# Optimization experiments

Hardware: AMD Instinct MI355X
Metric: run time of the kernel (lower is better)

Reference implementation:

```python
import jax, jax.numpy as jnp
import numpy as np

B, S, D, H, DFF = 2, 2048, 1024, 16, 4096
DK = D // H


def _layer_norm(x, g, b, eps=1e-5):
    mu = jnp.mean(x, axis=-1, keepdims=True)
    var = jnp.mean((x - mu) ** 2, axis=-1, keepdims=True)
    return (x - mu) / jnp.sqrt(var + eps) * g + b


def setup_inputs() -> dict:
    key = jax.random.key(0)
    ks = jax.random.split(key, 12)
    w = lambda k, shape: jax.random.normal(k, shape, jnp.float32) * 0.02
    return {
        "x": jax.random.normal(ks[0], (B, S, D), jnp.float32),
        "mask": jnp.tril(jnp.ones((1, 1, S, S), jnp.int32)),  # causal tgt mask
        "Wq": w(ks[1], (D, D)), "bq": jnp.zeros((D,), jnp.float32),
        "Wk": w(ks[2], (D, D)), "bk": jnp.zeros((D,), jnp.float32),
        "Wv": w(ks[3], (D, D)), "bv": jnp.zeros((D,), jnp.float32),
        "Wo": w(ks[4], (D, D)), "bo": jnp.zeros((D,), jnp.float32),
        "W1": w(ks[5], (D, DFF)), "b1": jnp.zeros((DFF,), jnp.float32),
        "W2": w(ks[6], (DFF, D)), "b2": jnp.zeros((D,), jnp.float32),
        "g1": jnp.ones((D,), jnp.float32), "be1": jnp.zeros((D,), jnp.float32),
        "g2": jnp.ones((D,), jnp.float32), "be2": jnp.zeros((D,), jnp.float32),
    }


def reference(x, mask, Wq, bq, Wk, bk, Wv, bv, Wo, bo, W1, b1, W2, b2, g1, be1, g2, be2):
    b, s, d = x.shape
    h, dk = H, DK
    split = lambda t: t.reshape(b, s, h, dk).transpose(0, 2, 1, 3)  # [b,h,s,dk]
    q = split(x @ Wq + bq)
    k = split(x @ Wk + bk)
    v = split(x @ Wv + bv)
    scores = jnp.einsum("bhqd,bhkd->bhqk", q, k) / jnp.sqrt(jnp.float32(dk))
    # ALiBi: slope_h = (2**(8/H))**-(h+1); bias[h,i,j] = slope_h * (j - i)
    slopes = (2.0 ** (8.0 / h)) ** (-jnp.arange(1, h + 1, dtype=jnp.float32))
    rel = (jnp.arange(s)[None, :] - jnp.arange(s)[:, None]).astype(jnp.float32)
    scores = scores + slopes[:, None, None] * rel[None]  # [1? broadcast b,h,s,s]
    scores = jnp.where(mask == 0, jnp.float32(-1e9), scores)
    probs = jax.nn.softmax(scores, axis=-1)
    attn = jnp.einsum("bhqk,bhkd->bhqd", probs, v)
    attn = attn.transpose(0, 2, 1, 3).reshape(b, s, d) @ Wo + bo
    x = _layer_norm(x + attn, g1, be1)
    ff = jax.nn.relu(x @ W1 + b1) @ W2 + b2
    return _layer_norm(x + ff, g2, be2)
```

## Files before the change

### kernel.cpp

```cpp
#include <hip/hip_runtime.h>
#include <stdint.h>

typedef unsigned short u16;
typedef __bf16 bf16x8 __attribute__((ext_vector_type(8)));
typedef float f32x4 __attribute__((ext_vector_type(4)));
typedef float f32x16 __attribute__((ext_vector_type(16)));
typedef unsigned int uint2v __attribute__((ext_vector_type(2)));

#define S_LEN 2048
#define D_MODEL 1024

struct TrueT  { static constexpr bool value = true;  };
struct FalseT { static constexpr bool value = false; };

__device__ __forceinline__ u16 f2b(float f) {
    uint32_t u = __float_as_uint(f);
    u += 0x7FFFu + ((u >> 16) & 1u);
    return (u16)(u >> 16);
}

__device__ __forceinline__ uint32_t pk2(float a, float b) {
    union { struct { __bf16 l, h; } s; uint32_t u; } c;
    c.s.l = (__bf16)a; c.s.h = (__bf16)b; return c.u;
}

__device__ __forceinline__ float fexp2(float x) {
#if __has_builtin(__builtin_amdgcn_exp2f)
    return __builtin_amdgcn_exp2f(x);
#else
    return exp2f(x);
#endif
}

__device__ __forceinline__ uint2v plswap(uint32_t a, uint32_t b) {
#if __has_builtin(__builtin_amdgcn_permlane32_swap)
    return __builtin_amdgcn_permlane32_swap(a, b, false, false);
#else
    uint2v r;
    uint32_t pa = (uint32_t)__shfl_xor((int)a, 32, 64);
    uint32_t pb = (uint32_t)__shfl_xor((int)b, 32, 64);
    const int hi = (threadIdx.x & 63) >> 5;
    r[0] = hi ? pb : a;
    r[1] = hi ? b : pa;
    return r;
#endif
}
__device__ __forceinline__ float xhalf_max(float x) {
    uint2v r = plswap(__float_as_uint(x), __float_as_uint(x));
    return fmaxf(__uint_as_float(r[0]), __uint_as_float(r[1]));
}
__device__ __forceinline__ float xhalf_add(float x) {
    uint2v r = plswap(__float_as_uint(x), __float_as_uint(x));
    return __uint_as_float(r[0]) + __uint_as_float(r[1]);
}

__device__ __forceinline__ void gl16(const void* g, void* l) {
    __builtin_amdgcn_global_load_lds(
        (const __attribute__((address_space(1))) void*)g,
        (__attribute__((address_space(3))) void*)l, 16, 0, 0);
}

__global__ __launch_bounds__(256) void k_convert_bf16(
    const float* __restrict__ in, u16* __restrict__ out, int n)
{
    int i = (blockIdx.x * 256 + threadIdx.x) * 4;
    if (i >= n) return;
    float4 v = *reinterpret_cast<const float4*>(in + i);
    ushort4 o;
    o.x = f2b(v.x); o.y = f2b(v.y); o.z = f2b(v.z); o.w = f2b(v.w);
    *reinterpret_cast<ushort4*>(out + i) = o;
}

__global__ __launch_bounds__(256) void k_transpose_w(
    const float* __restrict__ W, u16* __restrict__ WT, int K, int N)
{
    __shared__ float tile[32][33];
    const int nt = blockIdx.x, kt = blockIdx.y;
    const int tx = threadIdx.x & 31, ty = threadIdx.x >> 5;
#pragma unroll
    for (int i = 0; i < 4; ++i)
        tile[ty + i * 8][tx] = W[(long)(kt * 32 + ty + i * 8) * N + nt * 32 + tx];
    __syncthreads();
#pragma unroll
    for (int i = 0; i < 4; ++i)
        WT[(long)(nt * 32 + ty + i * 8) * K + kt * 32 + tx] = f2b(tile[tx][ty + i * 8]);
}

template <int MODE>
__global__ __launch_bounds__(256) void k_gemm(
    const u16* __restrict__ A, const u16* __restrict__ BT,
    const float* __restrict__ bias, const float* __restrict__ bias2,
    const float* __restrict__ bias3,
    u16* __restrict__ outb, float* __restrict__ outf,
    int M, int N, int K, int va, int vb)
{
    __shared__ u16 As[2][128 * 32];
    __shared__ u16 Bs[2][128 * 32];
    const int t = threadIdx.x;
    const int lane = t & 63, wid = t >> 6;
    const int wm = wid >> 1, wn = wid & 1;
    const int lr = lane & 15, lg = lane >> 4;

    const int GX = gridDim.x, GY = gridDim.y;
    const int dd = blockIdx.y * GX + blockIdx.x;
    const int xcd = dd & 7, ii = dd >> 3;
    const int hb = GY / va, wb = GX / vb;
    const int pr = xcd / vb, pc = xcd % vb;
    const int by = pr * hb + ii / wb;
    const int bx = pc * wb + ii % wb;
    const int m0 = by * 128, n0 = bx * 128;

    const int Kc = K / (int)gridDim.z;
    const long koff = (long)blockIdx.z * Kc;

    f32x4 acc[4][4];
#pragma unroll
    for (int i = 0; i < 4; ++i)
#pragma unroll
        for (int j = 0; j < 4; ++j) acc[i][j] = (f32x4){0.f, 0.f, 0.f, 0.f};

    const int r0 = t >> 2;
    const int ce = (t & 3) * 8;
    const u16* pA0 = A + (long)(m0 + r0) * K + ce + koff;
    const u16* pA1 = A + (long)(m0 + r0 + 64) * K + ce + koff;
    const u16* pB0 = BT + (long)(n0 + r0) * K + ce + koff;
    const u16* pB1 = BT + (long)(n0 + r0 + 64) * K + ce + koff;

    auto STAGE = [&](int buf, int k0) {
        u16* aw = &As[buf][wid * 512];
        u16* bw = &Bs[buf][wid * 512];
        gl16(pA0 + k0, aw);
        gl16(pA1 + k0, aw + 2048);
        gl16(pB0 + k0, bw);
        gl16(pB1 + k0, bw + 2048);
    };

    STAGE(0, 0);
    __syncthreads();
    int cur = 0;
    for (int k0 = 0; k0 < Kc; k0 += 32) {
        if (k0 + 32 < Kc) STAGE(cur ^ 1, k0 + 32);
        bf16x8 af[4], bfr[4];
#pragma unroll
        for (int i = 0; i < 4; ++i)
            af[i] = *reinterpret_cast<const bf16x8*>(&As[cur][(wm * 64 + i * 16 + lr) * 32 + lg * 8]);
#pragma unroll
        for (int j = 0; j < 4; ++j)
            bfr[j] = *reinterpret_cast<const bf16x8*>(&Bs[cur][(wn * 64 + j * 16 + lr) * 32 + lg * 8]);
#pragma unroll
        for (int i = 0; i < 4; ++i)
#pragma unroll
            for (int j = 0; j < 4; ++j)
                acc[i][j] = __builtin_amdgcn_mfma_f32_16x16x32_bf16(af[i], bfr[j], acc[i][j], 0, 0, 0);
        __syncthreads();
        cur ^= 1;
    }

    const long zoff = (long)blockIdx.z * M * N;
#pragma unroll
    for (int i = 0; i < 4; ++i) {
#pragma unroll
        for (int j = 0; j < 4; ++j) {
            const int n = n0 + wn * 64 + j * 16 + lr;
            float bn = 0.f;
            if (MODE == 0)
                bn = (n < 1024) ? bias[n] : (n < 2048) ? bias2[n - 1024] : bias3[n - 2048];
            else if (MODE == 2)
                bn = bias[n];
#pragma unroll
            for (int r = 0; r < 4; ++r) {
                const int m = m0 + wm * 64 + i * 16 + lg * 4 + r;
                float v = acc[i][j][r] + bn;
                if (MODE == 0) {
                    const int b = m >> 11, s = m & 2047;
                    const int which = n >> 10, nn = n & 1023;
                    const int h = nn >> 6, dk = nn & 63;
                    const long bhb = (long)(b * 16 + h) * (2048L * 64);
                    const int s32 = s >> 5, sr = s & 31;
                    long addr;
                    if (which < 2) {
                        addr = bhb + (long)s32 * 2048 + (dk >> 4) * 512 +
                               ((dk >> 3) & 1) * 256 + sr * 8 + (dk & 7);
                    } else {
                        addr = bhb + (long)s32 * 2048 + (dk >> 5) * 1024 +
                               ((sr >> 4) & 1) * 512 + ((sr >> 3) & 1) * 256 +
                               (dk & 31) * 8 + (sr & 7);
                    }
                    outb[(long)which * (32L * 2048 * 64) + addr] = f2b(v);
                } else if (MODE == 2) {
                    outb[(long)m * N + n] = f2b(fmaxf(v, 0.f));
                } else {
                    outf[zoff + (long)m * N + n] = v;
                }
            }
        }
    }
}

__global__ __launch_bounds__(512, 2) void k_gemm8(
    const u16* __restrict__ A, const u16* __restrict__ BT,
    const float* __restrict__ bias, u16* __restrict__ outb,
    int M, int N, int K, int va, int vb)
{
    __shared__ u16 As[2][2][8192];
    __shared__ u16 Bs[2][2][8192];
    const int t = threadIdx.x;
    const int lane = t & 63, wid = t >> 6;
    const int wm = wid >> 2, wn = wid & 3;
    const int lr = lane & 15, lg = lane >> 4;

    const int GX = gridDim.x, GY = gridDim.y;
    const int dd = blockIdx.y * GX + blockIdx.x;
    const int xcd = dd & 7, ii = dd >> 3;
    const int hb = GY / va, wb = GX / vb;
    const int by = (xcd / vb) * hb + ii / wb;
    const int bx = (xcd % vb) * wb + ii % wb;
    const int m0 = by * 256, n0 = bx * 256;

    const int NT = K >> 6;

    auto STAGEU = [&](const u16* __restrict__ P, int rbase, u16* lds_unit,
                      int tt, int kh) {
        const int ko = tt * 64 + kh * 32;
#pragma unroll
        for (int s = 0; s < 2; ++s) {
            const int c = wid * 64 + lane + s * 512;
            const int op = c * 16;
            const int row = op >> 6;
            const int kg = ((op >> 4) & 3) ^ (row & 3);
            gl16(P + (long)(rbase + row) * K + ko + kg * 8,
                 (char*)lds_unit + op);
        }
    };
    auto RD = [&](const u16* unit, int rb) -> bf16x8 {
        const int row = rb + lr;
        const int op = (row * 64 + lg * 16) ^ ((row & 3) << 4);
        return *reinterpret_cast<const bf16x8*>((const char*)unit + op);
    };

    f32x4 acc[8][4];
#pragma unroll
    for (int i = 0; i < 8; ++i)
#pragma unroll
        for (int j = 0; j < 4; ++j) acc[i][j] = (f32x4){0.f, 0.f, 0.f, 0.f};

    STAGEU(A, m0, &As[0][0][0], 0, 0);
    STAGEU(BT, n0, &Bs[0][0][0], 0, 0);
    STAGEU(A, m0, &As[0][1][0], 0, 1);
    STAGEU(BT, n0, &Bs[0][1][0], 0, 1);
    STAGEU(A, m0, &As[1][0][0], 1, 0);
    STAGEU(BT, n0, &Bs[1][0][0], 1, 0);
    asm volatile("s_waitcnt vmcnt(0)" ::: "memory");
    __builtin_amdgcn_s_barrier();

    for (int tt = 0; tt < NT; ++tt) {
        const int sl = tt & 1;
        bf16x8 af[4], bfr[4];

#pragma unroll
        for (int rf = 0; rf < 4; ++rf)
            af[rf] = RD(&As[sl][0][0], wm * 128 + rf * 16);
#pragma unroll
        for (int cf = 0; cf < 4; ++cf)
            bfr[cf] = RD(&Bs[sl][0][0], wn * 64 + cf * 16);
        if (tt + 1 < NT) STAGEU(A, m0, &As[sl ^ 1][1][0], tt + 1, 1);
        __builtin_amdgcn_s_setprio(1);
#pragma unroll
        for (int cf = 0; cf < 4; ++cf)
#pragma unroll
            for (int rf = 0; rf < 4; ++rf)
                acc[rf][cf] = __builtin_amdgcn_mfma_f32_16x16x32_bf16(af[rf], bfr[cf], acc[rf][cf], 0, 0, 0);
        __builtin_amdgcn_s_setprio(0);
        __builtin_amdgcn_s_barrier();

#pragma unroll
        for (int rf = 0; rf < 4; ++rf)
            af[rf] = RD(&As[sl][0][0], wm * 128 + 64 + rf * 16);
        if (tt + 1 < NT) STAGEU(BT, n0, &Bs[sl ^ 1][1][0], tt + 1, 1);
        __builtin_amdgcn_s_setprio(1);
#pragma unroll
        for (int cf = 0; cf < 4; ++cf)
#pragma unroll
            for (int rf = 0; rf < 4; ++rf)
                acc[4 + rf][cf] = __builtin_amdgcn_mfma_f32_16x16x32_bf16(af[rf], bfr[cf], acc[4 + rf][cf], 0, 0, 0);
        __builtin_amdgcn_s_setprio(0);
        asm volatile("s_waitcnt vmcnt(8)" ::: "memory");
        __builtin_amdgcn_s_barrier();

#pragma unroll
        for (int rf = 0; rf < 4; ++rf)
            af[rf] = RD(&As[sl][1][0], wm * 128 + rf * 16);
#pragma unroll
        for (int cf = 0; cf < 4; ++cf)
            bfr[cf] = RD(&Bs[sl][1][0], wn * 64 + cf * 16);
        if (tt + 2 < NT) STAGEU(A, m0, &As[sl][0][0], tt + 2, 0);
        __builtin_amdgcn_s_setprio(1);
#pragma unroll
        for (int cf = 0; cf < 4; ++cf)
#pragma unroll
            for (int rf = 0; rf < 4; ++rf)
                acc[rf][cf] = __builtin_amdgcn_mfma_f32_16x16x32_bf16(af[rf], bfr[cf], acc[rf][cf], 0, 0, 0);
        __builtin_amdgcn_s_setprio(0);
        __builtin_amdgcn_s_barrier();

#pragma unroll
        for (int rf = 0; rf < 4; ++rf)
            af[rf] = RD(&As[sl][1][0], wm * 128 + 64 + rf * 16);
        if (tt + 2 < NT) STAGEU(BT, n0, &Bs[sl][0][0], tt + 2, 0);
        __builtin_amdgcn_s_setprio(1);
#pragma unroll
        for (int cf = 0; cf < 4; ++cf)
#pragma unroll
            for (int rf = 0; rf < 4; ++rf)
                acc[4 + rf][cf] = __builtin_amdgcn_mfma_f32_16x16x32_bf16(af[rf], bfr[cf], acc[4 + rf][cf], 0, 0, 0);
        __builtin_amdgcn_s_setprio(0);
        asm volatile("s_waitcnt vmcnt(8)" ::: "memory");
        __builtin_amdgcn_s_barrier();
    }

#pragma unroll
    for (int fr = 0; fr < 8; ++fr)
#pragma unroll
        for (int cf = 0; cf < 4; ++cf) {
            const int n = n0 + wn * 64 + cf * 16 + lr;
            const float bn = bias[n];
#pragma unroll
            for (int r = 0; r < 4; ++r) {
                const int m = m0 + wm * 128 + fr * 16 + lg * 4 + r;
                outb[(long)m * N + n] = f2b(fmaxf(acc[fr][cf][r] + bn, 0.f));
            }
        }
}

__global__ __launch_bounds__(256, 3) void k_attn4(
    const u16* __restrict__ qg, const u16* __restrict__ kg,
    const u16* __restrict__ vtg, u16* __restrict__ attnb)
{
    __shared__ float Ol[4][32][68];
    __shared__ float Ml[4][32];
    __shared__ float Ll[4][32];

    const int t = threadIdx.x;
    const int lane = t & 63, w = t >> 6;
    const int qc = lane & 31, hi = lane >> 5;
    const int bid = blockIdx.x;
    const int xcd = bid & 7, slot = bid >> 3;
    const int bh = xcd * 4 + (slot & 3);
    const int pr = slot >> 2;
    const int b = bh >> 4, h = bh & 15;
    const float slope2 = fexp2(-0.5f * (float)(h + 1)) * 1.44269504f;
    const float SC = 0.18033688f;
    const long base = (long)bh * (S_LEN * 64L);

    const u16* kptr = kg + base + lane * 8;
    const u16* vptr = vtg + base + lane * 8;
    const u16* qptr = qg + base + lane * 8;

#define LOADK(S, DST) {                                                   \
        const u16* kr_ = kptr + (long)(S) * 2048;                         \
        DST[0] = *reinterpret_cast<const bf16x8*>(kr_);                   \
        DST[1] = *reinterpret_cast<const bf16x8*>(kr_ + 512);             \
        DST[2] = *reinterpret_cast<const bf16x8*>(kr_ + 1024);            \
        DST[3] = *reinterpret_cast<const bf16x8*>(kr_ + 1536); }

    for (int pi = 0; pi < 2; ++pi) {
        const int qt = pi ? pr : 63 - pr;
        const int q_abs = qt * 32 + qc;

        bf16x8 qf[4];
        {
            const u16* qt_ = qptr + (long)qt * 2048;
#pragma unroll
            for (int ds = 0; ds < 4; ++ds)
                qf[ds] = *reinterpret_cast<const bf16x8*>(qt_ + ds * 512);
        }

        f32x16 oacc[2];
#pragma unroll
        for (int i = 0; i < 16; ++i) { oacc[0][i] = 0.f; oacc[1][i] = 0.f; }
        float m = -1e30f, l = 0.f;

        const int nsub = qt + 1;
        const int L = (nsub + 3) >> 2;
        const int s_beg = w * L;
        const int s_end = min(s_beg + L, nsub);
        const bool has_diag = (s_beg < s_end) && (s_end == nsub);
        const int e_un = has_diag ? s_end - 1 : s_end;

        bf16x8 kf[4];

        auto SUBTILE = [&](int s, int nxt, auto MASKC) {
            constexpr bool MASK = decltype(MASKC)::value;
            const int k0 = s * 32;
            f32x16 st;
#pragma unroll
            for (int i = 0; i < 16; ++i) st[i] = 0.f;
#pragma unroll
            for (int ds = 0; ds < 4; ++ds)
                st = __builtin_amdgcn_mfma_f32_32x32x16_bf16(kf[ds], qf[ds], st, 0, 0, 0);
            if (nxt >= 0) LOADK(nxt, kf);
            bf16x8 vf[2][2];
            {
                const u16* vt_ = vptr + (long)s * 2048;
#pragma unroll
                for (int dh = 0; dh < 2; ++dh)
#pragma unroll
                    for (int ks = 0; ks < 2; ++ks)
                        vf[dh][ks] = *reinterpret_cast<const bf16x8*>(
                            vt_ + dh * 1024 + ks * 512);
            }

            const float b0 = slope2 * (float)(k0 - q_abs + 4 * hi);
#pragma unroll
            for (int r = 0; r < 16; ++r) {
                const int roff = (r & 3) + 8 * (r >> 2);
                float xx = fmaf(st[r], SC, fmaf((float)roff, slope2, b0));
                if (MASK) {
                    const int kabs = k0 + roff + 4 * hi;
                    xx = (kabs > q_abs) ? -1e30f : xx;
                }
                st[r] = xx;
            }
            float mt[8];
#pragma unroll
            for (int r = 0; r < 8; ++r) mt[r] = fmaxf(st[2 * r], st[2 * r + 1]);
#pragma unroll
            for (int r = 0; r < 4; ++r) mt[r] = fmaxf(mt[r], mt[r + 4]);
            mt[0] = fmaxf(mt[0], mt[2]); mt[1] = fmaxf(mt[1], mt[3]);
            float mloc = xhalf_max(fmaxf(mt[0], mt[1]));

            if (!__all(mloc <= m + 11.5416f)) {
                const float mnew = fmaxf(m, mloc);
                const float corr = fexp2(m - mnew);
                m = mnew;
                l *= corr;
#pragma unroll
                for (int i = 0; i < 16; ++i) { oacc[0][i] *= corr; oacc[1][i] *= corr; }
            }

#pragma unroll
            for (int r = 0; r < 16; ++r) st[r] = fexp2(st[r] - m);
            float pt[8];
#pragma unroll
            for (int r = 0; r < 8; ++r) pt[r] = st[2 * r] + st[2 * r + 1];
#pragma unroll
            for (int r = 0; r < 4; ++r) pt[r] = pt[r] + pt[r + 4];
            pt[0] += pt[2]; pt[1] += pt[3];
            l += xhalf_add(pt[0] + pt[1]);

            bf16x8 pa[2];
#pragma unroll
            for (int g2 = 0; g2 < 2; ++g2) {
                uint32_t o0 = pk2(st[8 * g2 + 0], st[8 * g2 + 1]);
                uint32_t o1 = pk2(st[8 * g2 + 2], st[8 * g2 + 3]);
                uint32_t o2 = pk2(st[8 * g2 + 4], st[8 * g2 + 5]);
                uint32_t o3 = pk2(st[8 * g2 + 6], st[8 * g2 + 7]);
                uint2v ra = plswap(o0, o2);
                uint2v rb = plswap(o1, o3);
                union { uint32_t wd[4]; bf16x8 v; } c;
                c.wd[0] = ra[0]; c.wd[1] = rb[0]; c.wd[2] = ra[1]; c.wd[3] = rb[1];
                pa[g2] = c.v;
            }
#pragma unroll
            for (int ks = 0; ks < 2; ++ks)
#pragma unroll
                for (int dh = 0; dh < 2; ++dh)
                    oacc[dh] = __builtin_amdgcn_mfma_f32_32x32x16_bf16(vf[dh][ks], pa[ks], oacc[dh], 0, 0, 0);
        };

        int s = s_beg;
        if (s < s_end) LOADK(s, kf);
        for (; s < e_un; ++s)
            SUBTILE(s, (s + 1 < s_end) ? s + 1 : -1, FalseT{});
        if (has_diag)
            SUBTILE(qt, -1, TrueT{});

#pragma unroll
        for (int dh = 0; dh < 2; ++dh)
#pragma unroll
            for (int g = 0; g < 4; ++g) {
                float4 o4 = make_float4(oacc[dh][4 * g + 0], oacc[dh][4 * g + 1],
                                        oacc[dh][4 * g + 2], oacc[dh][4 * g + 3]);
                *reinterpret_cast<float4*>(&Ol[w][qc][dh * 32 + g * 8 + hi * 4]) = o4;
            }
        if (hi == 0) { Ml[w][qc] = m; Ll[w][qc] = l; }
        __syncthreads();

        {
            const int q = t >> 3, dg = t & 7;
            const float m0v = Ml[0][q], m1v = Ml[1][q], m2v = Ml[2][q], m3v = Ml[3][q];
            const float M = fmaxf(fmaxf(m0v, m1v), fmaxf(m2v, m3v));
            float wgt[4];
            wgt[0] = fexp2(m0v - M); wgt[1] = fexp2(m1v - M);
            wgt[2] = fexp2(m2v - M); wgt[3] = fexp2(m3v - M);
            const float lsum = wgt[0] * Ll[0][q] + wgt[1] * Ll[1][q] +
                               wgt[2] * Ll[2][q] + wgt[3] * Ll[3][q];
            float acc8[8];
#pragma unroll
            for (int e = 0; e < 8; ++e) acc8[e] = 0.f;
#pragma unroll
            for (int w4 = 0; w4 < 4; ++w4) {
                const float wg = wgt[w4];
#pragma unroll
                for (int e = 0; e < 8; ++e)
                    acc8[e] += wg * Ol[w4][q][dg * 8 + e];
            }
            const float inv = 1.0f / lsum;
            u16 ob[8];
#pragma unroll
            for (int e = 0; e < 8; ++e) ob[e] = f2b(acc8[e] * inv);
            *reinterpret_cast<uint4*>(
                &attnb[((long)b * S_LEN + qt * 32 + q) * 1024 + h * 64 + dg * 8]) =
                *reinterpret_cast<uint4*>(&ob[0]);
        }
        __syncthreads();
    }
#undef LOADK
}

__global__ __launch_bounds__(256) void k_ln(
    const float* __restrict__ P0, const float* __restrict__ P1,
    const float* __restrict__ resid, const float* __restrict__ pbias,
    const float* __restrict__ g, const float* __restrict__ be,
    float* __restrict__ outf, u16* __restrict__ outb, int writeb)
{
    __shared__ float red[2][4];
    const int row = blockIdx.x, t = threadIdx.x;
    const long o = (long)row * 1024 + t * 4;
    float4 a0 = *reinterpret_cast<const float4*>(P0 + o);
    float4 a1 = *reinterpret_cast<const float4*>(P1 + o);
    float4 rr = *reinterpret_cast<const float4*>(resid + o);
    float4 pb = *reinterpret_cast<const float4*>(pbias + t * 4);
    float4 vv;
    vv.x = a0.x + a1.x + rr.x + pb.x;
    vv.y = a0.y + a1.y + rr.y + pb.y;
    vv.z = a0.z + a1.z + rr.z + pb.z;
    vv.w = a0.w + a1.w + rr.w + pb.w;
    float s = vv.x + vv.y + vv.z + vv.w;
    float sq = vv.x * vv.x + vv.y * vv.y + vv.z * vv.z + vv.w * vv.w;
#pragma unroll
    for (int off = 1; off < 64; off <<= 1) {
        s += __shfl_xor(s, off, 64);
        sq += __shfl_xor(sq, off, 64);
    }
    const int w = t >> 6;
    if ((t & 63) == 0) { red[0][w] = s; red[1][w] = sq; }
    __syncthreads();
    s = red[0][0] + red[0][1] + red[0][2] + red[0][3];
    sq = red[1][0] + red[1][1] + red[1][2] + red[1][3];
    const float mu = s * (1.f / 1024.f);
    const float var = sq * (1.f / 1024.f) - mu * mu;
    const float rs = rsqrtf(var + 1e-5f);
    float4 gv = *reinterpret_cast<const float4*>(&g[t * 4]);
    float4 bv = *reinterpret_cast<const float4*>(&be[t * 4]);
    float4 ov;
    ov.x = (vv.x - mu) * rs * gv.x + bv.x;
    ov.y = (vv.y - mu) * rs * gv.y + bv.y;
    ov.z = (vv.z - mu) * rs * gv.z + bv.z;
    ov.w = (vv.w - mu) * rs * gv.w + bv.w;
    *reinterpret_cast<float4*>(&outf[o]) = ov;
    if (writeb) {
        ushort4 ob;
        ob.x = f2b(ov.x); ob.y = f2b(ov.y); ob.z = f2b(ov.z); ob.w = f2b(ov.w);
        *reinterpret_cast<ushort4*>(&outb[o]) = ob;
    }
}

extern "C" void kernel_launch(void* const* d_in, const int* in_sizes, int n_in,
                              void* d_out, int out_size, void* d_ws, size_t ws_size,
                              hipStream_t stream)
{
    const float* x  = (const float*)d_in[0];
    const float* Wq = (const float*)d_in[2];  const float* bq = (const float*)d_in[3];
    const float* Wk = (const float*)d_in[4];  const float* bk = (const float*)d_in[5];
    const float* Wv = (const float*)d_in[6];  const float* bv = (const float*)d_in[7];
    const float* Wo = (const float*)d_in[8];  const float* bo = (const float*)d_in[9];
    const float* W1 = (const float*)d_in[10]; const float* b1 = (const float*)d_in[11];
    const float* W2 = (const float*)d_in[12]; const float* b2 = (const float*)d_in[13];
    const float* g1 = (const float*)d_in[14]; const float* be1 = (const float*)d_in[15];
    const float* g2 = (const float*)d_in[16]; const float* be2 = (const float*)d_in[17];
    float* out = (float*)d_out;

    char* ws = (char*)d_ws;
    const size_t MB = 1 << 20;
    u16* XB   = (u16*)(ws + 0 * MB);
    u16* QKVT = (u16*)(ws + 8 * MB);
    u16* WOT  = (u16*)(ws + 14 * MB);
    u16* W1T  = (u16*)(ws + 16 * MB);
    u16* W2T  = (u16*)(ws + 96 * MB);
    u16* QKV  = (u16*)(ws + 32 * MB);
    u16* AT   = (u16*)(ws + 64 * MB);
    float* OP = (float*)(ws + 32 * MB);
    float* Y1 = (float*)(ws + 0 * MB);
    u16* Y1B  = (u16*)(ws + 64 * MB);
    u16* Hb   = (u16*)(ws + 24 * MB);
    float* FP = (float*)(ws + 56 * MB);

    u16* Qb = QKV;
    u16* Kb = QKV + 32L * 2048 * 64;
    u16* Vb = QKV + 2 * 32L * 2048 * 64;

    dim3 blk(256);

    k_convert_bf16<<<dim3(4096), blk, 0, stream>>>(x, XB, 4096 * 1024);
    k_transpose_w<<<dim3(32, 32), blk, 0, stream>>>(Wq, QKVT, 1024, 1024);
    k_transpose_w<<<dim3(32, 32), blk, 0, stream>>>(Wk, QKVT + 1024L * 1024, 1024, 1024);
    k_transpose_w<<<dim3(32, 32), blk, 0, stream>>>(Wv, QKVT + 2048L * 1024, 1024, 1024);
    k_transpose_w<<<dim3(32, 32), blk, 0, stream>>>(Wo, WOT, 1024, 1024);
    k_transpose_w<<<dim3(128, 32), blk, 0, stream>>>(W1, W1T, 1024, 4096);
    k_transpose_w<<<dim3(32, 128), blk, 0, stream>>>(W2, W2T, 4096, 1024);

    k_gemm<0><<<dim3(24, 32), blk, 0, stream>>>(XB, QKVT, bq, bk, bv,
                                                QKV, nullptr, 4096, 3072, 1024, 4, 2);

    k_attn4<<<dim3(1024), blk, 0, stream>>>(Qb, Kb, Vb, AT);

    k_gemm<1><<<dim3(8, 32, 2), blk, 0, stream>>>(AT, WOT, nullptr, nullptr, nullptr,
                                                  nullptr, OP, 4096, 1024, 1024, 4, 2);
    k_ln<<<dim3(4096), blk, 0, stream>>>(OP, OP + 4096L * 1024, x, bo,
                                         g1, be1, Y1, Y1B, 1);
    k_gemm8<<<dim3(16, 16), dim3(512), 0, stream>>>(Y1B, W1T, b1, Hb,
                                                    4096, 4096, 1024, 2, 4);
    k_gemm<1><<<dim3(8, 32, 2), blk, 0, stream>>>(Hb, W2T, nullptr, nullptr, nullptr,
                                                  nullptr, FP, 4096, 1024, 4096, 4, 2);
    k_ln<<<dim3(4096), blk, 0, stream>>>(FP, FP + 4096L * 1024, Y1, b2,
                                         g2, be2, out, nullptr, 0);
}
```

Measured before the change: 234.1 us.

## Add 512-thread split-K GEMM with 256x128 tiles for output and FFN2 projections

Introduces k_gemm8n, a 512-thread, 8-wave GEMM with 256x128 block tiles and split-K over gridDim.z that writes fp32 partials, and uses it for the Wo and W2 projections in place of the 256-thread k_gemm<1>. It also changes the LDS swizzle in k_gemm8 from row&3 to (row>>1)&3 to reduce bank conflicts on the 64-byte row layout. The goal is better MFMA utilisation and latency hiding for the N=1024 GEMMs. The trade-off is fewer, larger blocks (256 total) and higher register and LDS use per block.

```diff
diff --git a/kernel.cpp b/kernel.cpp
--- a/kernel.cpp
+++ b/kernel.cpp
@@ -227,14 +227,14 @@
             const int c = wid * 64 + lane + s * 512;
             const int op = c * 16;
             const int row = op >> 6;
-            const int kg = ((op >> 4) & 3) ^ (row & 3);
+            const int kg = ((op >> 4) & 3) ^ ((row >> 1) & 3);
             gl16(P + (long)(rbase + row) * K + ko + kg * 8,
                  (char*)lds_unit + op);
         }
     };
     auto RD = [&](const u16* unit, int rb) -> bf16x8 {
         const int row = rb + lr;
-        const int op = (row * 64 + lg * 16) ^ ((row & 3) << 4);
+        const int op = (row * 64 + lg * 16) ^ (((row >> 1) & 3) << 4);
         return *reinterpret_cast<const bf16x8*>((const char*)unit + op);
     };
 
@@ -328,6 +328,127 @@
             for (int r = 0; r < 4; ++r) {
                 const int m = m0 + wm * 128 + fr * 16 + lg * 4 + r;
                 outb[(long)m * N + n] = f2b(fmaxf(acc[fr][cf][r] + bn, 0.f));
+            }
+        }
+}
+
+__global__ __launch_bounds__(512, 2) void k_gemm8n(
+    const u16* __restrict__ A, const u16* __restrict__ BT,
+    float* __restrict__ outf, int M, int N, int K, int va, int vb)
+{
+    __shared__ u16 As[2][2][8192];
+    __shared__ u16 Bs[2][2][4096];
+    const int t = threadIdx.x;
+    const int lane = t & 63, wid = t >> 6;
+    const int wm = wid >> 1, wn = wid & 1;
+    const int lr = lane & 15, lg = lane >> 4;
+
+    const int GX = gridDim.x, GY = gridDim.y;
+    const int dd = blockIdx.y * GX + blockIdx.x;
+    const int xcd = dd & 7, ii = dd >> 3;
+    const int hb = GY / va, wb = GX / vb;
+    const int by = (xcd / vb) * hb + ii / wb;
+    const int bx = (xcd % vb) * wb + ii % wb;
+    const int m0 = by * 256, n0 = bx * 128;
+
+    const int Kc = K / (int)gridDim.z;
+    const long koff = (long)blockIdx.z * Kc;
+    const int NT = Kc >> 6;
+
+    auto STAGEA = [&](u16* lds_unit, int tt, int kh) {
+        const int ko = tt * 64 + kh * 32;
+#pragma unroll
+        for (int s = 0; s < 2; ++s) {
+            const int c = wid * 64 + lane + s * 512;
+            const int op = c * 16;
+            const int row = op >> 6;
+            const int kg = ((op >> 4) & 3) ^ ((row >> 1) & 3);
+            gl16(A + (long)(m0 + row) * K + koff + ko + kg * 8,
+                 (char*)lds_unit + op);
+        }
+    };
+    auto STAGEB = [&](u16* lds_unit, int tt, int kh) {
+        const int ko = tt * 64 + kh * 32;
+        const int c = wid * 64 + lane;
+        const int op = c * 16;
+        const int row = op >> 6;
+        const int kg = ((op >> 4) & 3) ^ ((row >> 1) & 3);
+        gl16(BT + (long)(n0 + row) * K + koff + ko + kg * 8,
+             (char*)lds_unit + op);
+    };
+    auto RD = [&](const u16* unit, int rb) -> bf16x8 {
+        const int row = rb + lr;
+        const int op = (row * 64 + lg * 16) ^ (((row >> 1) & 3) << 4);
+        return *reinterpret_cast<const bf16x8*>((const char*)unit + op);
+    };
+
+    f32x4 acc[4][4];
+#pragma unroll
+    for (int i = 0; i < 4; ++i)
+#pragma unroll
+        for (int j = 0; j < 4; ++j) acc[i][j] = (f32x4){0.f, 0.f, 0.f, 0.f};
+
+    STAGEA(&As[0][0][0], 0, 0); STAGEB(&Bs[0][0][0], 0, 0);
+    STAGEA(&As[0][1][0], 0, 1); STAGEB(&Bs[0][1][0], 0, 1);
+    STAGEA(&As[1][0][0], 1, 0); STAGEB(&Bs[1][0][0], 1, 0);
+    asm volatile("s_waitcnt vmcnt(0)" ::: "memory");
+    __builtin_amdgcn_s_barrier();
+
+    for (int tt = 0; tt < NT; ++tt) {
+        const int sl = tt & 1;
+        bf16x8 af[4], bfr[4];
+
+#pragma unroll
+        for (int rf = 0; rf < 4; ++rf)
+            af[rf] = RD(&As[sl][0][0], wm * 64 + rf * 16);
+#pragma unroll
+        for (int cf = 0; cf < 4; ++cf)
+            bfr[cf] = RD(&Bs[sl][0][0], wn * 64 + cf * 16);
+        if (tt + 1 < NT) {
+            STAGEA(&As[sl ^ 1][1][0], tt + 1, 1);
+            STAGEB(&Bs[sl ^ 1][1][0], tt + 1, 1);
+        }
+        __builtin_amdgcn_s_setprio(1);
+#pragma unroll
+        for (int cf = 0; cf < 4; ++cf)
+#pragma unroll
+            for (int rf = 0; rf < 4; ++rf)
+                acc[rf][cf] = __builtin_amdgcn_mfma_f32_16x16x32_bf16(af[rf], bfr[cf], acc[rf][cf], 0, 0, 0);
+        __builtin_amdgcn_s_setprio(0);
+        asm volatile("s_waitcnt vmcnt(6)" ::: "memory");
+        __builtin_amdgcn_s_barrier();
+
+#pragma unroll
+        for (int rf = 0; rf < 4; ++rf)
+            af[rf] = RD(&As[sl][1][0], wm * 64 + rf * 16);
+#pragma unroll
+        for (int cf = 0; cf < 4; ++cf)
+            bfr[cf] = RD(&Bs[sl][1][0], wn * 64 + cf * 16);
+        if (tt + 2 < NT) {
+            STAGEA(&As[sl][0][0], tt + 2, 0);
+            STAGEB(&Bs[sl][0][0], tt + 2, 0);
+        }
+        __builtin_amdgcn_s_setprio(1);
+#pragma unroll
+        for (int cf = 0; cf < 4; ++cf)
+#pragma unroll
+            for (int rf = 0; rf < 4; ++rf)
+                acc[rf][cf] = __builtin_amdgcn_mfma_f32_16x16x32_bf16(af[rf], bfr[cf], acc[rf][cf], 0, 0, 0);
+        __builtin_amdgcn_s_setprio(0);
+        asm volatile("s_waitcnt vmcnt(6)" ::: "memory");
+        __builtin_amdgcn_s_barrier();
+    }
+
+    const long zoff = (long)blockIdx.z * M * N;
+#pragma unroll
+    for (int fr = 0; fr < 4; ++fr)
+#pragma unroll
+        for (int cf = 0; cf < 4; ++cf) {
+            const int n = n0 + wn * 64 + cf * 16 + lr;
+#pragma unroll
+            for (int r = 0; r < 4; ++r) {
+                const int m = m0 + wm * 64 + fr * 16 + lg * 4 + r;
+                outf[zoff + (long)m * N + n] = acc[fr][cf][r];
             }
         }
 }
@@ -615,14 +736,14 @@
 
     k_attn4<<<dim3(1024), blk, 0, stream>>>(Qb, Kb, Vb, AT);
 
-    k_gemm<1><<<dim3(8, 32, 2), blk, 0, stream>>>(AT, WOT, nullptr, nullptr, nullptr,
-                                                  nullptr, OP, 4096, 1024, 1024, 4, 2);
+    k_gemm8n<<<dim3(8, 16, 2), dim3(512), 0, stream>>>(AT, WOT, OP,
+                                                       4096, 1024, 1024, 2, 4);
     k_ln<<<dim3(4096), blk, 0, stream>>>(OP, OP + 4096L * 1024, x, bo,
                                          g1, be1, Y1, Y1B, 1);
     k_gemm8<<<dim3(16, 16), dim3(512), 0, stream>>>(Y1B, W1T, b1, Hb,
                                                     4096, 4096, 1024, 2, 4);
-    k_gemm<1><<<dim3(8, 32, 2), blk, 0, stream>>>(Hb, W2T, nullptr, nullptr, nullptr,
-                                                  nullptr, FP, 4096, 1024, 4096, 4, 2);
+    k_gemm8n<<<dim3(8, 16, 2), dim3(512), 0, stream>>>(Hb, W2T, FP,
+                                                       4096, 1024, 4096, 2, 4);
     k_ln<<<dim3(4096), blk, 0, stream>>>(FP, FP + 4096L * 1024, Y1, b2,
                                          g2, be2, out, nullptr, 0);
 }
```

Result: faster. 222.9 us (-4.8%).
